# Optimization experiments

Measured on AMD Instinct MI355X. Metric: run time of the kernel, lower is better.

## Reference

```python
import jax, jax.numpy as jnp
import numpy as np

N = 8192      # nodes
E = 262144    # edges (avg degree 32)
D = 128       # embed dim
F = 128       # input feature dim
H = 128       # GCN hidden
C = 7         # classes
EPS = 1e-4    # sample_bias for concrete noise


def setup_inputs() -> dict:
    key = jax.random.key(0)
    ks = jax.random.split(key, 10)
    x = jax.random.normal(ks[0], (N, F), jnp.float32)
    embed = jax.random.normal(ks[1], (N, D), jnp.float32)
    row = jax.random.randint(ks[2], (E,), 0, N, jnp.int64)
    col = jax.random.randint(ks[3], (E,), 0, N, jnp.int64)
    adj_data = jnp.ones((E,), jnp.float32)
    # uniform noise in (bias, 1-bias) as in concrete_sample(training=True)
    noise = jax.random.uniform(ks[4], (E,), jnp.float32, EPS, 1.0 - EPS)
    tmp = jnp.ones((1,), jnp.float32)  # temperature beta
    W1e = jax.random.normal(ks[5], (3 * D, 64), jnp.float32) * 0.05
    b1e = jnp.zeros((64,), jnp.float32)
    W2e = jax.random.normal(ks[6], (64, 1), jnp.float32) * 0.05
    b2e = jnp.zeros((1,), jnp.float32)
    Wg0 = jax.random.normal(ks[7], (F, H), jnp.float32) * 0.05
    Wg1 = jax.random.normal(ks[8], (H, C), jnp.float32) * 0.05
    return {"x": x, "embed": embed, "adj_data": adj_data, "noise": noise,
            "tmp": tmp, "W1e": W1e, "b1e": b1e, "W2e": W2e, "b2e": b2e,
            "Wg0": Wg0, "Wg1": Wg1, "row": row, "col": col, "nodeid": 5}


def reference(x, embed, adj_data, noise, tmp, W1e, b1e, W2e, b2e, Wg0, Wg1,
              row, col, nodeid):
    # gather node embeddings per edge + self node embedding, concat -> [E, 3D]
    f1 = embed[row]
    f2 = embed[col]
    selfemb = jnp.broadcast_to(embed[nodeid][None, :], (f1.shape[0], D))
    f12self = jnp.concatenate([f1, f2, selfemb], axis=-1)
    # 2-layer explainer MLP -> per-edge logit
    h = jax.nn.relu(f12self @ W1e + b1e)
    log_alpha = (h @ W2e + b2e).reshape(-1)  # [E]
    # concrete-sigmoid reparameterization (training=True path, noise supplied)
    gate_inputs = (jnp.log(noise) - jnp.log1p(-noise) + log_alpha) / tmp[0]
    values = jax.nn.sigmoid(gate_inputs)
    # scatter edge gates and adjacency values into dense [N, N]
    mask = jnp.zeros((N, N), jnp.float32).at[row, col].add(values)
    adj = jnp.zeros((N, N), jnp.float32).at[row, col].add(adj_data)
    # symmetrize mask, apply to adjacency, zero the diagonal
    sym_mask = (mask + mask.T) * 0.5
    masked_adj = adj * sym_mask * (1.0 - jnp.eye(N, dtype=jnp.float32))
    # wrapped GNN: 2-layer GCN
    h1 = jax.nn.relu(masked_adj @ (x @ Wg0))
    out = masked_adj @ (h1 @ Wg1)
    node_pred = out[nodeid]  # [C]
    return jax.nn.softmax(node_pred, axis=0)
```

## Files before the change

kernel.cpp:

```cpp
#include <hip/hip_runtime.h>
#include <hip/hip_bf16.h>
#include <math.h>

#define NNODES 8192
#define DIM 128
#define SMAX 128
#define HSIZE 16384
#define LDA2 68

__device__ __forceinline__ int detect64(const void* rowp) {
    const long long* p = (const long long*)rowp;
    int is64 = 1;
#pragma unroll
    for (int i = 0; i < 4; i++) {
        long long v = p[i];
        if (v < 0 || v >= NNODES) is64 = 0;
    }
    return is64;
}

__device__ __forceinline__ int edge_idx(const void* p, int e, int idx64) {
    if (idx64) return (int)((const long long*)p)[e];
    return ((const int*)p)[e];
}

__device__ __forceinline__ int hash_insert(unsigned int* hashK, unsigned int key1) {
    unsigned int h = (key1 * 2654435761u) & (HSIZE - 1);
    for (;;) {
        unsigned int prev = atomicCAS(&hashK[h], 0u, key1);
        if (prev == 0u || prev == key1) return (int)h;
        h = (h + 1) & (HSIZE - 1);
    }
}


__global__ __launch_bounds__(256) void k_zero(float4* z, int n4) {
    int i = blockIdx.x * blockDim.x + threadIdx.x;
    if (i < n4) z[i] = make_float4(0.f, 0.f, 0.f, 0.f);
}

__global__ __launch_bounds__(256) void k_dense(
        const float* embed, const float* W1e, const float* b1e,
        const int* nodep, const void* rowp, const void* colp, const float* adjd,
        float* U, float* V, float* cself,
        int* flags, float* cnt0, int* nbr, int* slotmap,
        float* hzero, int nhz, int E) {
    int bid = blockIdx.x;
    int t = threadIdx.x;
    int gid = bid * 256 + t;
    int nodeid = nodep[0];
    int tile = bid >> 1;
    int colh = bid & 1;

    __shared__ float At[128 * LDA2];
    __shared__ float Wl[128 * LDA2];
    __shared__ float semb[DIM];

    for (int i = gid; i < nhz; i += 256 * 256) hzero[i] = 0.f;

    const float* Asrc = embed + (size_t)tile * 64 * DIM;
    for (int i = t; i < 64 * DIM; i += 256)
        At[(i & 127) * LDA2 + (i >> 7)] = Asrc[i];
    int doff = colh * 128;
    for (int i = t; i < 128 * 64; i += 256)
        Wl[(i >> 6) * LDA2 + (i & 63)] = W1e[(size_t)(doff + (i >> 6)) * 64 + (i & 63)];
    if (bid == 0 && t < DIM) semb[t] = embed[(size_t)nodeid * DIM + t];
    __syncthreads();

    int rg = t & 15;
    int cg = t >> 4;
    float acc[4][4];
#pragma unroll
    for (int i = 0; i < 4; i++)
#pragma unroll
        for (int j = 0; j < 4; j++) acc[i][j] = 0.f;

#pragma unroll 4
    for (int d = 0; d < DIM; d++) {
        float4 a4 = *(const float4*)&At[d * LDA2 + rg * 4];
        float4 w4 = *(const float4*)&Wl[d * LDA2 + cg * 4];
        const float* ap = &a4.x;
        const float* wp = &w4.x;
#pragma unroll
        for (int i = 0; i < 4; i++)
#pragma unroll
            for (int j = 0; j < 4; j++)
                acc[i][j] = fmaf(ap[i], wp[j], acc[i][j]);
    }

    float* o = colh ? V : U;
    int n0 = tile * 64;
#pragma unroll
    for (int i = 0; i < 4; i++)
        *(float4*)&o[(size_t)(n0 + rg * 4 + i) * 64 + cg * 4] =
            make_float4(acc[i][0], acc[i][1], acc[i][2], acc[i][3]);

    if (bid == 0 && t < 64) {
        float a = b1e[t];
        for (int d = 0; d < DIM; d++)
            a += semb[d] * W1e[(size_t)(2 * DIM + d) * 64 + t];
        cself[t] = a;
    }

    int idx64 = detect64(rowp);
    for (int e = gid; e < E; e += 256 * 256) {
        int r = edge_idx(rowp, e, idx64);
        if (r != nodeid) continue;
        int c = edge_idx(colp, e, idx64);
        if (c == nodeid) continue;
        atomicAdd(&cnt0[c], adjd[e]);
        if (atomicCAS((unsigned int*)&slotmap[c], 0u, 0xFFFFFFFFu) == 0u) {
            int s = atomicAdd(&flags[1], 1);
            if (s < SMAX) {
                nbr[s] = c;
                __hip_atomic_store(&slotmap[c], s + 1, __ATOMIC_RELAXED,
                                   __HIP_MEMORY_SCOPE_AGENT);
            }
        }
    }
}

__global__ __launch_bounds__(1024) void k_gates(
        const float* adjd, const float* noise, const float* tmp,
        const float* W2e, const float* b2e,
        const void* rowp, const void* colp, const int* nodep,
        const float* U, const float* V, const float* cself,
        const int* slotmap,
        unsigned int* hashK, float* hashC, float* hashF, float* hashR,
        float* f0s, float* r0s, int E) {
    int idx64 = detect64(rowp);
    int nodeid = nodep[0];
    int e = blockIdx.x * blockDim.x + threadIdx.x;
    if (e >= E) return;
    int r = edge_idx(rowp, e, idx64);
    int c = edge_idx(colp, e, idx64);
    if (r == c) return;
    int spr = slotmap[r];
    int spc = slotmap[c];
    bool fr = spr > 0, fc = spc > 0;
    if (!fr && !fc) return;
    float la = b2e[0];
    const float4* u4 = (const float4*)(U + (size_t)r * 64);
    const float4* v4 = (const float4*)(V + (size_t)c * 64);
    const float4* c4 = (const float4*)cself;
    const float4* w4 = (const float4*)W2e;
#pragma unroll
    for (int d = 0; d < 16; d++) {
        float4 uu = u4[d], vv = v4[d], cc = c4[d], ww = w4[d];
        float h0 = uu.x + vv.x + cc.x;
        float h1 = uu.y + vv.y + cc.y;
        float h2 = uu.z + vv.z + cc.z;
        float h3 = uu.w + vv.w + cc.w;
        la += (h0 > 0.f ? h0 : 0.f) * ww.x + (h1 > 0.f ? h1 : 0.f) * ww.y
            + (h2 > 0.f ? h2 : 0.f) * ww.z + (h3 > 0.f ? h3 : 0.f) * ww.w;
    }
    float nz = noise[e];
    float gi = (logf(nz) - log1pf(-nz) + la) / tmp[0];
    float v = 1.f / (1.f + expf(-gi));
    if (fr) {
        int sr = spr - 1;
        unsigned int key1 = ((unsigned int)(sr << 13) | (unsigned int)c) + 1u;
        int idx = hash_insert(hashK, key1);
        atomicAdd(&hashC[idx], adjd[e]);
        atomicAdd(&hashF[idx], v);
        if (c == nodeid) atomicAdd(&r0s[sr], v);
    }
    if (fc) {
        int sc = spc - 1;
        unsigned int key1 = ((unsigned int)(sc << 13) | (unsigned int)r) + 1u;
        int idx = hash_insert(hashK, key1);
        atomicAdd(&hashR[idx], v);
        if (r == nodeid) atomicAdd(&f0s[sc], v);
    }
}

__global__ __launch_bounds__(1024) void k_hagg(
        const unsigned int* hashK, const float* hashC, const float* hashF,
        const float* hashR, const float* x, float* xagg) {
    int gid = blockIdx.x * blockDim.x + threadIdx.x;
    int group = gid >> 7;
    int tg = gid & 127;
    int ngroups = (256 * 1024) >> 7;
    for (int entry = group; entry < HSIZE; entry += ngroups) {
        unsigned int key1 = hashK[entry];
        if (key1 == 0u) continue;
        float wgt = hashC[entry] * (hashF[entry] + hashR[entry]) * 0.5f;
        if (wgt == 0.f) continue;
        unsigned int key = key1 - 1u;
        int s = (int)(key >> 13);
        int k = (int)(key & 8191u);
        atomicAdd(&xagg[(size_t)s * DIM + tg], wgt * x[(size_t)k * DIM + tg]);
    }
}

__global__ __launch_bounds__(128) void k_final(
        const int* flags, const float* xagg, const float* cnt0, const int* nbr,
        const float* f0s, const float* r0s, const float* Wg0, const float* Wg1,
        float* glogits, int* done, float* out) {
    int b = blockIdx.x, t = threadIdx.x;
    int ns = flags[1]; if (ns > SMAX) ns = SMAX;
    if (b < ns) {
        __shared__ float xs[DIM];
        __shared__ float pacc[2][7];
        xs[t] = xagg[(size_t)b * DIM + t];
        __syncthreads();
        float h = 0.f;
        for (int d = 0; d < DIM; d++) h = fmaf(xs[d], Wg0[d * DIM + t], h);
        h = h > 0.f ? h : 0.f;
        int wave = t >> 6, lane = t & 63;
        float part[7];
        for (int c = 0; c < 7; c++) {
            float p = h * Wg1[t * 7 + c];
            for (int o = 32; o >= 1; o >>= 1) p += __shfl_xor(p, o, 64);
            part[c] = p;
        }
        if (lane == 0)
            for (int c = 0; c < 7; c++) pacc[wave][c] = part[c];
        __syncthreads();
        if (t == 0) {
            float a0 = cnt0[nbr[b]] * (f0s[b] + r0s[b]) * 0.5f;
            for (int c = 0; c < 7; c++)
                atomicAdd(&glogits[c * 16], a0 * (pacc[0][c] + pacc[1][c]));
        }
    }
    __syncthreads();
    __shared__ int lastb;
    if (t == 0) {
        __threadfence();
        int old = __hip_atomic_fetch_add(done, 1, __ATOMIC_ACQ_REL,
                                         __HIP_MEMORY_SCOPE_AGENT);
        lastb = (old == SMAX - 1) ? 1 : 0;
    }
    __syncthreads();
    if (!lastb || t != 0) return;
    __builtin_amdgcn_fence(__ATOMIC_ACQUIRE, "agent");
    float v[7], m = -1e30f, ssum = 0.f;
    for (int c = 0; c < 7; c++) {
        v[c] = __hip_atomic_load(&glogits[c * 16], __ATOMIC_RELAXED,
                                 __HIP_MEMORY_SCOPE_AGENT);
        if (v[c] > m) m = v[c];
    }
    for (int c = 0; c < 7; c++) { v[c] = expf(v[c] - m); ssum += v[c]; }
    for (int c = 0; c < 7; c++) out[c] = v[c] / ssum;
}

extern "C" void kernel_launch(void* const* d_in, const int* in_sizes, int n_in,
                              void* d_out, int out_size, void* d_ws, size_t ws_size,
                              hipStream_t stream) {
    const float* x     = (const float*)d_in[0];
    const float* embed = (const float*)d_in[1];
    const float* adjd  = (const float*)d_in[2];
    const float* noise = (const float*)d_in[3];
    const float* tmp   = (const float*)d_in[4];
    const float* W1e   = (const float*)d_in[5];
    const float* b1e   = (const float*)d_in[6];
    const float* W2e   = (const float*)d_in[7];
    const float* b2e   = (const float*)d_in[8];
    const float* Wg0   = (const float*)d_in[9];
    const float* Wg1   = (const float*)d_in[10];
    const void*  rowp  = d_in[11];
    const void*  colp  = d_in[12];
    const int*   nodep = (const int*)d_in[13];
    int E = in_sizes[3];

    char* w = (char*)d_ws;
    size_t off = 0;
    auto alloc = [&](size_t bytes) -> char* {
        char* p = w + off;
        off = (off + bytes + 255) & ~(size_t)255;
        return p;
    };
    float*        cself   = (float*)alloc(64 * 4);
    int*          nbr     = (int*)  alloc(SMAX * 4);
    float*        U       = (float*)alloc((size_t)NNODES * 64 * 4);
    float*        V       = (float*)alloc((size_t)NNODES * 64 * 4);
    char*         zstart  = w + off;
    int*          flags   = (int*)  alloc(256);
    float*        glogits = (float*)alloc(512);
    int*          slotmap = (int*)  alloc((size_t)NNODES * 4);
    float*        cnt0    = (float*)alloc((size_t)NNODES * 4);
    float*        f0s     = (float*)alloc(SMAX * 4);
    float*        r0s     = (float*)alloc(SMAX * 4);
    size_t zbytes  = (size_t)((w + off) - zstart);
    unsigned int* hashK   = (unsigned int*)alloc((size_t)HSIZE * 4);
    float*        hashC   = (float*)alloc((size_t)HSIZE * 4);
    float*        hashF   = (float*)alloc((size_t)HSIZE * 4);
    float*        hashR   = (float*)alloc((size_t)HSIZE * 4);
    float*        xagg    = (float*)alloc((size_t)SMAX * DIM * 4);
    int nhz = HSIZE * 4 + SMAX * DIM;
    int n4 = (int)(zbytes / 16);

    k_zero<<<(n4 + 255) / 256, 256, 0, stream>>>((float4*)zstart, n4);
    k_dense<<<256, 256, 0, stream>>>(embed, W1e, b1e, nodep, rowp, colp, adjd,
                                     U, V, cself, flags, cnt0, nbr, slotmap,
                                     (float*)hashK, nhz, E);
    k_gates<<<E / 1024, 1024, 0, stream>>>(adjd, noise, tmp, W2e, b2e,
                                           rowp, colp, nodep, U, V, cself,
                                           slotmap, hashK, hashC, hashF, hashR,
                                           f0s, r0s, E);
    k_hagg<<<256, 1024, 0, stream>>>(hashK, hashC, hashF, hashR, x, xagg);
    k_final<<<SMAX, 128, 0, stream>>>(flags, xagg, cnt0, nbr, f0s, r0s,
                                      Wg0, Wg1, glogits, &flags[2],
                                      (float*)d_out);
}
```

Before: 48.21 us.

## Fuse hash aggregation and final GCN/softmax into one kernel via last-block pattern

Measured after the change: 72.52 us. 1.5x slower.

```diff
diff --git a/kernel.cpp b/kernel.cpp
--- a/kernel.cpp
+++ b/kernel.cpp
@@ -174,12 +174,16 @@
     }
 }
 
-__global__ __launch_bounds__(1024) void k_hagg(
-        const unsigned int* hashK, const float* hashC, const float* hashF,
-        const float* hashR, const float* x, float* xagg) {
-    int gid = blockIdx.x * blockDim.x + threadIdx.x;
+__global__ __launch_bounds__(1024) void k_tail(
+        const int* flags, const unsigned int* hashK, const float* hashC,
+        const float* hashF, const float* hashR, const float* x,
+        const float* cnt0, const int* nbr, const float* f0s, const float* r0s,
+        const float* Wg0, const float* Wg1,
+        float* xagg, int* done, float* out) {
+    int bid = blockIdx.x, t = threadIdx.x;
+    int gid = bid * 1024 + t;
     int group = gid >> 7;
-    int tg = gid & 127;
+    int tg = t & 127;
     int ngroups = (256 * 1024) >> 7;
     for (int entry = group; entry < HSIZE; entry += ngroups) {
         unsigned int key1 = hashK[entry];
@@ -191,57 +195,58 @@
         int k = (int)(key & 8191u);
         atomicAdd(&xagg[(size_t)s * DIM + tg], wgt * x[(size_t)k * DIM + tg]);
     }
-}
-
-__global__ __launch_bounds__(128) void k_final(
-        const int* flags, const float* xagg, const float* cnt0, const int* nbr,
-        const float* f0s, const float* r0s, const float* Wg0, const float* Wg1,
-        float* glogits, int* done, float* out) {
-    int b = blockIdx.x, t = threadIdx.x;
-    int ns = flags[1]; if (ns > SMAX) ns = SMAX;
-    if (b < ns) {
-        __shared__ float xs[DIM];
-        __shared__ float pacc[2][7];
-        xs[t] = xagg[(size_t)b * DIM + t];
-        __syncthreads();
-        float h = 0.f;
-        for (int d = 0; d < DIM; d++) h = fmaf(xs[d], Wg0[d * DIM + t], h);
-        h = h > 0.f ? h : 0.f;
-        int wave = t >> 6, lane = t & 63;
-        float part[7];
-        for (int c = 0; c < 7; c++) {
-            float p = h * Wg1[t * 7 + c];
-            for (int o = 32; o >= 1; o >>= 1) p += __shfl_xor(p, o, 64);
-            part[c] = p;
-        }
-        if (lane == 0)
-            for (int c = 0; c < 7; c++) pacc[wave][c] = part[c];
-        __syncthreads();
-        if (t == 0) {
-            float a0 = cnt0[nbr[b]] * (f0s[b] + r0s[b]) * 0.5f;
-            for (int c = 0; c < 7; c++)
-                atomicAdd(&glogits[c * 16], a0 * (pacc[0][c] + pacc[1][c]));
-        }
-    }
     __syncthreads();
     __shared__ int lastb;
     if (t == 0) {
         __threadfence();
         int old = __hip_atomic_fetch_add(done, 1, __ATOMIC_ACQ_REL,
                                          __HIP_MEMORY_SCOPE_AGENT);
-        lastb = (old == SMAX - 1) ? 1 : 0;
+        lastb = (old == 255) ? 1 : 0;
     }
     __syncthreads();
-    if (!lastb || t != 0) return;
+    if (!lastb) return;
     __builtin_amdgcn_fence(__ATOMIC_ACQUIRE, "agent");
-    float v[7], m = -1e30f, ssum = 0.f;
-    for (int c = 0; c < 7; c++) {
-        v[c] = __hip_atomic_load(&glogits[c * 16], __ATOMIC_RELAXED,
-                                 __HIP_MEMORY_SCOPE_AGENT);
-        if (v[c] > m) m = v[c];
-    }
-    for (int c = 0; c < 7; c++) { v[c] = expf(v[c] - m); ssum += v[c]; }
-    for (int c = 0; c < 7; c++) out[c] = v[c] / ssum;
+
+    __shared__ float sacc[7];
+    __shared__ float xs[8][DIM];
+    if (t < 7) sacc[t] = 0.f;
+    int ns = flags[1]; if (ns > SMAX) ns = SMAX;
+    int j = t & 127;
+    int sl = t >> 7;
+    int lane = t & 63;
+    for (int s0 = 0; s0 < ns; s0 += 8) {
+        __syncthreads();
+        for (int i = t; i < 8 * DIM; i += 1024) {
+            int s = s0 + (i >> 7);
+            xs[i >> 7][i & 127] = (s < ns) ? xagg[(size_t)s * DIM + (i & 127)] : 0.f;
+        }
+        __syncthreads();
+        int s = s0 + sl;
+        float contrib[7] = {0.f, 0.f, 0.f, 0.f, 0.f, 0.f, 0.f};
+        if (s < ns) {
+            float h = 0.f;
+            for (int d = 0; d < DIM; d++)
+                h = fmaf(xs[sl][d], Wg0[d * DIM + j], h);
+            h = h > 0.f ? h : 0.f;
+            float a0 = cnt0[nbr[s]] * (f0s[s] + r0s[s]) * 0.5f;
+            float ah = a0 * h;
+#pragma unroll
+            for (int c = 0; c < 7; c++) contrib[c] = ah * Wg1[j * 7 + c];
+        }
+#pragma unroll
+        for (int c = 0; c < 7; c++) {
+            float p = contrib[c];
+            for (int o = 32; o >= 1; o >>= 1) p += __shfl_xor(p, o, 64);
+            if (lane == 0 && p != 0.f) atomicAdd(&sacc[c], p);
+        }
+    }
+    __syncthreads();
+    if (t == 0) {
+        float v[7], m = -1e30f, ssum = 0.f;
+        for (int c = 0; c < 7; c++) { v[c] = sacc[c]; if (v[c] > m) m = v[c]; }
+        for (int c = 0; c < 7; c++) { v[c] = expf(v[c] - m); ssum += v[c]; }
+        for (int c = 0; c < 7; c++) out[c] = v[c] / ssum;
+    }
 }
 
 extern "C" void kernel_launch(void* const* d_in, const int* in_sizes, int n_in,
@@ -276,7 +281,6 @@
     float*        V       = (float*)alloc((size_t)NNODES * 64 * 4);
     char*         zstart  = w + off;
     int*          flags   = (int*)  alloc(256);
-    float*        glogits = (float*)alloc(512);
     int*          slotmap = (int*)  alloc((size_t)NNODES * 4);
     float*        cnt0    = (float*)alloc((size_t)NNODES * 4);
     float*        f0s     = (float*)alloc(SMAX * 4);
@@ -298,8 +302,7 @@
                                            rowp, colp, nodep, U, V, cself,
                                            slotmap, hashK, hashC, hashF, hashR,
                                            f0s, r0s, E);
-    k_hagg<<<256, 1024, 0, stream>>>(hashK, hashC, hashF, hashR, x, xagg);
-    k_final<<<SMAX, 128, 0, stream>>>(flags, xagg, cnt0, nbr, f0s, r0s,
-                                      Wg0, Wg1, glogits, &flags[2],
-                                      (float*)d_out);
-}
+    k_tail<<<256, 1024, 0, stream>>>(flags, hashK, hashC, hashF, hashR, x,
+                                     cnt0, nbr, f0s, r0s, Wg0, Wg1,
+                                     xagg, &flags[2], (float*)d_out);
+}
```
